# Kernel tuning notes

Hardware: AMD Instinct MI355X
Metric: run time of the kernel (lower is better)

Reference implementation:

```python
import jax, jax.numpy as jnp
import numpy as np

B, S, D = 4, 2048, 1024


def setup_inputs() -> dict:
    key = jax.random.key(0)
    ks = jax.random.split(key, 9)
    scale = 1.0 / np.sqrt(D)
    v = jax.random.normal(ks[0], (B, S, D), dtype=jnp.float32)
    k = jax.random.normal(ks[1], (B, S, D), dtype=jnp.float32)
    q = jax.random.normal(ks[2], (B, S, D), dtype=jnp.float32)
    # causal boolean mask broadcast over batch: [B, S, S]
    mask = jnp.broadcast_to(jnp.tril(jnp.ones((S, S), dtype=bool)), (B, S, S))
    Wq = jax.random.normal(ks[3], (D, D), dtype=jnp.float32) * scale
    bq = jnp.zeros((D,), dtype=jnp.float32)
    Wk = jax.random.normal(ks[4], (D, D), dtype=jnp.float32) * scale
    bk = jnp.zeros((D,), dtype=jnp.float32)
    Wv = jax.random.normal(ks[5], (D, D), dtype=jnp.float32) * scale
    bv = jnp.zeros((D,), dtype=jnp.float32)
    return {"v": v, "k": k, "q": q, "mask": mask,
            "Wq": Wq, "bq": bq, "Wk": Wk, "bk": bk, "Wv": Wv, "bv": bv}


def reference(v, k, q, mask, Wq, bq, Wk, bk, Wv, bv):
    # Dense projections (flax Dense: x @ W + b)
    qp = jnp.einsum('bsd,de->bse', q, Wq) + bq
    kp = jnp.einsum('bsd,de->bse', k, Wk) + bk
    vp = jnp.einsum('bsd,de->bse', v, Wv) + bv
    inv_sqrt_d = jnp.float32(1.0 / np.sqrt(D))
    scores = jnp.einsum('bqd,bkd->bqk', qp, kp) * inv_sqrt_d  # [B,S,S]
    scores = jnp.where(mask, scores, jnp.float32(-1e10))
    attn = jax.nn.softmax(scores, axis=-1)
    return qp + jnp.einsum('bqk,bkd->bqd', attn, vp)
```

## Files before the change

kernel.cpp:

```cpp
#include <hip/hip_runtime.h>
#include <hip/hip_bf16.h>
#include <stdint.h>
#include <stddef.h>


using bf16 = __hip_bfloat16;
typedef __attribute__((ext_vector_type(8))) short short8;
typedef __attribute__((ext_vector_type(4))) float f32x4;

#define B_ 4
#define S_ 2048
#define D_ 1024
#define NTOK (B_ * S_)
#define NELEM ((size_t)NTOK * D_)

__device__ __forceinline__ float bits_to_f(unsigned short h) {
  union { unsigned int u; float f; } c;
  c.u = ((unsigned int)h) << 16;
  return c.f;
}

__device__ __forceinline__ void gld_lds16(const void* g, void* l) {
  __builtin_amdgcn_global_load_lds(
      (const __attribute__((address_space(1))) unsigned int*)g,
      (__attribute__((address_space(3))) unsigned int*)l, 16, 0, 0);
}

__global__ void detect_kernel(const unsigned short* __restrict__ qraw,
                              int* __restrict__ flag) {
  const int lane = threadIdx.x;
  const float v = fabsf(bits_to_f(qraw[2 * lane]));
  const bool sane = (v < 64.0f) && (v == 0.0f || v > 1e-30f);
  const unsigned long long m = __ballot(sane);
  if (lane == 0) *flag = (__popcll(m) >= 56) ? 1 : 0;
}

__global__ __launch_bounds__(256) void prep_kernel(
    const void* __restrict__ v, const void* __restrict__ k,
    const void* __restrict__ q,
    const void* __restrict__ Wq, const void* __restrict__ Wk,
    const void* __restrict__ Wv,
    bf16* __restrict__ X, bf16* __restrict__ WT,
    float* __restrict__ rowsum, const int* __restrict__ flag)
{
  __shared__ bf16 tbuf[32][33];
  const int bid = blockIdx.x;
  const int tid = threadIdx.x;
  const int mode = *flag;

  if (bid < 12288) {
    const int z = bid >> 12;
    const void* src = (z == 0) ? v : (z == 1) ? k : q;
    bf16* d = X + (size_t)z * NELEM;
    const size_t i = (size_t)(bid & 4095) * 256 + tid;
    if (mode) {
      ((uint4*)d)[i] = ((const uint4*)src)[i];
    } else {
      const float4 a = ((const float4*)src)[2 * i];
      const float4 b = ((const float4*)src)[2 * i + 1];
      __align__(16) bf16 t[8];
      t[0] = __float2bfloat16(a.x); t[1] = __float2bfloat16(a.y);
      t[2] = __float2bfloat16(a.z); t[3] = __float2bfloat16(a.w);
      t[4] = __float2bfloat16(b.x); t[5] = __float2bfloat16(b.y);
      t[6] = __float2bfloat16(b.z); t[7] = __float2bfloat16(b.w);
      ((uint4*)d)[i] = *(const uint4*)t;
    }
  } else if (bid < 15360) {
    const int t = bid - 12288;
    const int z = t >> 10;
    const int tt = t & 1023;
    const void* W = (z == 0) ? Wq : (z == 1) ? Wk : Wv;
    bf16* O = WT + (size_t)z * D_ * D_;
    const int bx = (tt & 31) * 32, by = (tt >> 5) * 32;
    const int tx = tid & 31, ty = tid >> 5;
#pragma unroll
    for (int i = 0; i < 32; i += 8) {
      const size_t idx = (size_t)(by + ty + i) * D_ + bx + tx;
      const float val = mode ? __bfloat162float(((const bf16*)W)[idx])
                             : ((const float*)W)[idx];
      tbuf[ty + i][tx] = __float2bfloat16(val);
    }
    __syncthreads();
#pragma unroll
    for (int i = 0; i < 32; i += 8)
      O[(size_t)(bx + ty + i) * D_ + by + tx] = tbuf[tx][ty + i];
  } else {
    rowsum[(bid - 15360) * 256 + tid] = 0.f;
  }
}

__device__ __forceinline__ void gemm128_core(
    const bf16* __restrict__ A, int lda, int m0,
    const bf16* __restrict__ Bt, int ldb, int n0,
    int kEnd, bf16* As, bf16* Bs, f32x4 acc[4][4])
{
  const int tid  = threadIdx.x;
  const int wave = tid >> 6;
  const int lane = tid & 63;
  const int wm = (wave & 1) * 64;
  const int wn = (wave >> 1) * 64;
  const int fr = lane & 15;
  const int q4 = lane >> 4;
  const int sw = fr & 7;
  const int srow = lane >> 3;
  const int scol = ((lane & 7) ^ (lane >> 3)) * 8;

  for (int k0 = 0; k0 < kEnd; k0 += 64) {
    __syncthreads();
#pragma unroll
    for (int i = 0; i < 4; ++i) {
      const int rb = (i * 4 + wave) * 8;
      gld_lds16(A  + (size_t)(m0 + rb + srow) * lda + k0 + scol, As + rb * 64);
      gld_lds16(Bt + (size_t)(n0 + rb + srow) * ldb + k0 + scol, Bs + rb * 64);
    }
    __syncthreads();
#pragma unroll
    for (int kk = 0; kk < 64; kk += 32) {
      const int c0 = (kk >> 3) + q4;
      const int coff = (c0 ^ sw) * 8;
      short8 a[4], b[4];
#pragma unroll
      for (int t = 0; t < 4; ++t) {
        a[t] = *(const short8*)(As + (wm + t * 16 + fr) * 64 + coff);
        b[t] = *(const short8*)(Bs + (wn + t * 16 + fr) * 64 + coff);
      }
#pragma unroll
      for (int mt = 0; mt < 4; ++mt)
#pragma unroll
        for (int nt = 0; nt < 4; ++nt)
          acc[mt][nt] = __builtin_amdgcn_mfma_f32_16x16x32_bf16(
              a[mt], b[nt], acc[mt][nt], 0, 0, 0);
    }
  }
}

__global__ __launch_bounds__(256) void proj_kernel(
    const bf16* __restrict__ xc,
    const bf16* __restrict__ WT,
    const void* __restrict__ bq, const void* __restrict__ bk,
    const void* __restrict__ bv,
    bf16* __restrict__ qp, bf16* __restrict__ kp, bf16* __restrict__ vpt,
    const int* __restrict__ flag)
{
  __shared__ bf16 As[128 * 64];
  __shared__ bf16 Bs[128 * 64];
  const int z = blockIdx.z;
  const bf16* A    = xc + (size_t)(z == 0 ? 2 : (z == 1 ? 1 : 0)) * NELEM;
  const void* bias = (z == 0) ? bq : (z == 1) ? bk : bv;
  const bf16* Bt = WT + (size_t)z * D_ * D_;
  const int m0 = blockIdx.x * 128, n0 = blockIdx.y * 128;
  const int mode = *flag;

  f32x4 acc[4][4] = {};
  gemm128_core(A, D_, m0, Bt, D_, n0, D_, As, Bs, acc);

  const int lane = threadIdx.x & 63, wave = threadIdx.x >> 6;
  const int wm = (wave & 1) * 64, wn = (wave >> 1) * 64;
  const int ccol = lane & 15, crow = (lane >> 4) * 4;
#pragma unroll
  for (int mt = 0; mt < 4; ++mt)
#pragma unroll
    for (int nt = 0; nt < 4; ++nt)
#pragma unroll
      for (int i = 0; i < 4; ++i) {
        const int m = m0 + wm + mt * 16 + crow + i;
        const int n = n0 + wn + nt * 16 + ccol;
        const float bval = mode ? __bfloat162float(((const bf16*)bias)[n])
                                : ((const float*)bias)[n];
        const float val = acc[mt][nt][i] + bval;
        if (z == 0)      qp[(size_t)m * D_ + n] = __float2bfloat16(val);
        else if (z == 1) kp[(size_t)m * D_ + n] = __float2bfloat16(val);
        else {
          const int b = m >> 11, s = m & (S_ - 1);
          vpt[((size_t)b * D_ + n) * S_ + s] = __float2bfloat16(val);
        }
      }
}

__global__ __launch_bounds__(256) void scores_kernel(
    const bf16* __restrict__ qp, const bf16* __restrict__ kp,
    bf16* __restrict__ sc, float* __restrict__ rowsum)
{
  const int m0 = blockIdx.x * 128, n0 = blockIdx.y * 128, bb = blockIdx.z;
  if (n0 > m0) return;
  __shared__ bf16 As[128 * 64];
  __shared__ bf16 Bs[128 * 64];
  const bf16* A  = qp + (size_t)bb * S_ * D_;
  const bf16* Bt = kp + (size_t)bb * S_ * D_;

  f32x4 acc[4][4] = {};
  gemm128_core(A, D_, m0, Bt, D_, n0, D_, As, Bs, acc);

  bf16* out = sc + (size_t)bb * S_ * S_;
  float* rs = rowsum + (size_t)bb * S_;
  const float scale = 0.03125f;
  const float MAXS = 8.0f;
  const int lane = threadIdx.x & 63, wave = threadIdx.x >> 6;
  const int wm = (wave & 1) * 64, wn = (wave >> 1) * 64;
  const int ccol = lane & 15, crow = (lane >> 4) * 4;
#pragma unroll
  for (int mt = 0; mt < 4; ++mt) {
#pragma unroll
    for (int i = 0; i < 4; ++i) {
      const int m = m0 + wm + mt * 16 + crow + i;
      float part = 0.f;
#pragma unroll
      for (int nt = 0; nt < 4; ++nt) {
        const int n = n0 + wn + nt * 16 + ccol;
        float p = 0.f;
        if (n <= m) {
          const bf16 pb = __float2bfloat16(__expf(acc[mt][nt][i] * scale - MAXS));
          p = __bfloat162float(pb);
          out[(size_t)m * S_ + n] = pb;
        } else {
          out[(size_t)m * S_ + n] = __float2bfloat16(0.f);
        }
        part += p;
      }
      part += __shfl_down(part, 8, 64);
      part += __shfl_down(part, 4, 64);
      part += __shfl_down(part, 2, 64);
      part += __shfl_down(part, 1, 64);
      if (ccol == 0) atomicAdd(&rs[m], part);
    }
  }
}

__global__ __launch_bounds__(256) void pv_kernel(
    const bf16* __restrict__ attn, const bf16* __restrict__ vpt,
    const bf16* __restrict__ qp, const float* __restrict__ rowsum,
    void* __restrict__ out, const int* __restrict__ flag)
{
  __shared__ bf16 As[128 * 64];
  __shared__ bf16 Bs[128 * 64];
  const int m0 = (15 - blockIdx.x) * 128;
  const int n0 = blockIdx.y * 128, bb = blockIdx.z;
  const bf16* A  = attn + (size_t)bb * S_ * S_;
  const bf16* Bt = vpt  + (size_t)bb * D_ * S_;
  const int mode = *flag;

  f32x4 acc[4][4] = {};
  gemm128_core(A, S_, m0, Bt, S_, n0, m0 + 128, As, Bs, acc);

  const bf16* qpb = qp + (size_t)bb * S_ * D_;
  const float* rs = rowsum + (size_t)bb * S_;
  const size_t obase = (size_t)bb * S_ * D_;
  const int lane = threadIdx.x & 63, wave = threadIdx.x >> 6;
  const int wm = (wave & 1) * 64, wn = (wave >> 1) * 64;
  const int ccol = lane & 15, crow = (lane >> 4) * 4;
#pragma unroll
  for (int mt = 0; mt < 4; ++mt)
#pragma unroll
    for (int i = 0; i < 4; ++i) {
      const int m = m0 + wm + mt * 16 + crow + i;
      const float inv = 1.f / rs[m];
#pragma unroll
      for (int nt = 0; nt < 4; ++nt) {
        const int n = n0 + wn + nt * 16 + ccol;
        const float val = acc[mt][nt][i] * inv +
                          __bfloat162float(qpb[(size_t)m * D_ + n]);
        const size_t idx = obase + (size_t)m * D_ + n;
        if (mode) ((bf16*)out)[idx] = __float2bfloat16(val);
        else      ((float*)out)[idx] = val;
      }
    }
}

extern "C" void kernel_launch(void* const* d_in, const int* in_sizes, int n_in,
                              void* d_out, int out_size, void* d_ws, size_t ws_size,
                              hipStream_t stream) {
  (void)in_sizes; (void)n_in; (void)out_size; (void)ws_size;
  const void* v  = d_in[0];
  const void* k  = d_in[1];
  const void* q  = d_in[2];
  const void* Wq = d_in[4];
  const void* bq = d_in[5];
  const void* Wk = d_in[6];
  const void* bk = d_in[7];
  const void* Wv = d_in[8];
  const void* bv = d_in[9];

  char* ws = (char*)d_ws;
  int*   flag   = (int*)ws;           ws += 256;
  float* rowsum = (float*)ws;         ws += (size_t)NTOK * 4;
  bf16* WT   = (bf16*)ws;             ws += (size_t)3 * D_ * D_ * 2;
  bf16* qp   = (bf16*)ws;             ws += NELEM * 2;
  bf16* kp   = (bf16*)ws;             ws += NELEM * 2;
  bf16* vpt  = (bf16*)ws;             ws += NELEM * 2;
  bf16* X    = (bf16*)ws;
  bf16* sc   = X;

  detect_kernel<<<dim3(1), dim3(64), 0, stream>>>((const unsigned short*)q, flag);
  prep_kernel<<<dim3(15392), dim3(256), 0, stream>>>(
      v, k, q, Wq, Wk, Wv, X, WT, rowsum, flag);
  proj_kernel<<<dim3(64, 8, 3), dim3(256), 0, stream>>>(
      X, WT, bq, bk, bv, qp, kp, vpt, flag);
  scores_kernel<<<dim3(16, 16, 4), dim3(256), 0, stream>>>(qp, kp, sc, rowsum);
  pv_kernel<<<dim3(16, 8, 4), dim3(256), 0, stream>>>(
      sc, vpt, qp, rowsum, d_out, flag);
}
```

Measured before the change: 390.6 us.

## Widen projection GEMM tile to 128x256 and compact causal scores grid

The projection GEMM now uses a 128x256 output tile per block, doubling per-wave accumulators so each A tile loaded into shared memory is reused across twice as many columns. The launch grid halves along N and launch bounds request two blocks per CU. Separately, the scores kernel launches only the lower-triangular tiles (544 blocks), mapping a linear index to (row, col) with a sqrt-based inverse, instead of launching a full grid where half the blocks exit immediately. The larger tile raises register and LDS pressure, which may reduce occupancy or cause spills.

```diff
diff --git a/kernel.cpp b/kernel.cpp
--- a/kernel.cpp
+++ b/kernel.cpp
@@ -134,7 +134,57 @@
   }
 }
 
-__global__ __launch_bounds__(256) void proj_kernel(
+__device__ __forceinline__ void gemm128x256_core(
+    const bf16* __restrict__ A, int lda, int m0,
+    const bf16* __restrict__ Bt, int ldb, int n0,
+    int kEnd, bf16* As, bf16* Bs, f32x4 acc[4][8])
+{
+  const int tid  = threadIdx.x;
+  const int wave = tid >> 6;
+  const int lane = tid & 63;
+  const int wm = (wave & 1) * 64;
+  const int wn = (wave >> 1) * 128;
+  const int fr = lane & 15;
+  const int q4 = lane >> 4;
+  const int sw = fr & 7;
+  const int srow = lane >> 3;
+  const int scol = ((lane & 7) ^ (lane >> 3)) * 8;
+
+  for (int k0 = 0; k0 < kEnd; k0 += 64) {
+    __syncthreads();
+#pragma unroll
+    for (int i = 0; i < 4; ++i) {
+      const int rb = (wave * 4 + i) * 8;
+      gld_lds16(A + (size_t)(m0 + rb + srow) * lda + k0 + scol, As + rb * 64);
+    }
+#pragma unroll
+    for (int i = 0; i < 8; ++i) {
+      const int rb = (wave * 8 + i) * 8;
+      gld_lds16(Bt + (size_t)(n0 + rb + srow) * ldb + k0 + scol, Bs + rb * 64);
+    }
+    __syncthreads();
+#pragma unroll
+    for (int kk = 0; kk < 64; kk += 32) {
+      const int c0 = (kk >> 3) + q4;
+      const int coff = (c0 ^ sw) * 8;
+      short8 a[4], b[8];
+#pragma unroll
+      for (int t = 0; t < 4; ++t)
+        a[t] = *(const short8*)(As + (wm + t * 16 + fr) * 64 + coff);
+#pragma unroll
+      for (int t = 0; t < 8; ++t)
+        b[t] = *(const short8*)(Bs + (wn + t * 16 + fr) * 64 + coff);
+#pragma unroll
+      for (int mt = 0; mt < 4; ++mt)
+#pragma unroll
+        for (int nt = 0; nt < 8; ++nt)
+          acc[mt][nt] = __builtin_amdgcn_mfma_f32_16x16x32_bf16(
+              a[mt], b[nt], acc[mt][nt], 0, 0, 0);
+    }
+  }
+}
+
+__global__ __launch_bounds__(256, 2) void proj_kernel(
     const bf16* __restrict__ xc,
     const bf16* __restrict__ WT,
     const void* __restrict__ bq, const void* __restrict__ bk,
@@ -143,24 +193,24 @@
     const int* __restrict__ flag)
 {
   __shared__ bf16 As[128 * 64];
-  __shared__ bf16 Bs[128 * 64];
+  __shared__ bf16 Bs[256 * 64];
   const int z = blockIdx.z;
   const bf16* A    = xc + (size_t)(z == 0 ? 2 : (z == 1 ? 1 : 0)) * NELEM;
   const void* bias = (z == 0) ? bq : (z == 1) ? bk : bv;
   const bf16* Bt = WT + (size_t)z * D_ * D_;
-  const int m0 = blockIdx.x * 128, n0 = blockIdx.y * 128;
+  const int m0 = blockIdx.x * 128, n0 = blockIdx.y * 256;
   const int mode = *flag;
 
-  f32x4 acc[4][4] = {};
-  gemm128_core(A, D_, m0, Bt, D_, n0, D_, As, Bs, acc);
+  f32x4 acc[4][8] = {};
+  gemm128x256_core(A, D_, m0, Bt, D_, n0, D_, As, Bs, acc);
 
   const int lane = threadIdx.x & 63, wave = threadIdx.x >> 6;
-  const int wm = (wave & 1) * 64, wn = (wave >> 1) * 64;
+  const int wm = (wave & 1) * 64, wn = (wave >> 1) * 128;
   const int ccol = lane & 15, crow = (lane >> 4) * 4;
 #pragma unroll
   for (int mt = 0; mt < 4; ++mt)
 #pragma unroll
-    for (int nt = 0; nt < 4; ++nt)
+    for (int nt = 0; nt < 8; ++nt)
 #pragma unroll
       for (int i = 0; i < 4; ++i) {
         const int m = m0 + wm + mt * 16 + crow + i;
@@ -181,8 +231,15 @@
     const bf16* __restrict__ qp, const bf16* __restrict__ kp,
     bf16* __restrict__ sc, float* __restrict__ rowsum)
 {
-  const int m0 = blockIdx.x * 128, n0 = blockIdx.y * 128, bb = blockIdx.z;
-  if (n0 > m0) return;
+  const int idx = blockIdx.x;
+  const int bb = idx & 3;
+  const int t = idx >> 2;
+  int mt_ = (int)((sqrtf(8.f * (float)t + 1.f) - 1.f) * 0.5f);
+  while ((mt_ + 1) * (mt_ + 2) / 2 <= t) ++mt_;
+  while (mt_ * (mt_ + 1) / 2 > t) --mt_;
+  const int nt_ = t - mt_ * (mt_ + 1) / 2;
+  const int m0 = mt_ * 128, n0 = nt_ * 128;
+
   __shared__ bf16 As[128 * 64];
   __shared__ bf16 Bs[128 * 64];
   const bf16* A  = qp + (size_t)bb * S_ * D_;
@@ -293,9 +350,9 @@
   detect_kernel<<<dim3(1), dim3(64), 0, stream>>>((const unsigned short*)q, flag);
   prep_kernel<<<dim3(15392), dim3(256), 0, stream>>>(
       v, k, q, Wq, Wk, Wv, X, WT, rowsum, flag);
-  proj_kernel<<<dim3(64, 8, 3), dim3(256), 0, stream>>>(
+  proj_kernel<<<dim3(64, 4, 3), dim3(256), 0, stream>>>(
       X, WT, bq, bk, bv, qp, kp, vpt, flag);
-  scores_kernel<<<dim3(16, 16, 4), dim3(256), 0, stream>>>(qp, kp, sc, rowsum);
+  scores_kernel<<<dim3(544), dim3(256), 0, stream>>>(qp, kp, sc, rowsum);
   pv_kernel<<<dim3(16, 8, 4), dim3(256), 0, stream>>>(
       sc, vpt, qp, rowsum, d_out, flag);
 }
```

Measured after the change: 391.7 us. No clear change (+0.3%).
